# Kernel optimization log

Hardware: AMD Instinct MI355X
Metric: run time of the kernel (lower is better)

Reference implementation:

```python
import jax, jax.numpy as jnp
import numpy as np

BETA = 0.25       # commit-loss weight (beta)
INIT_GAIN = 0.02  # trunc_normal std for codebook init
B, L, D = 4, 4096, 3
VOCAB = 8192


def setup_inputs() -> dict:
    key = jax.random.key(0)
    k1, k2 = jax.random.split(key)
    feats = jax.random.normal(k1, (B, L, D), dtype=jnp.float32)
    # frozen codebook (nn.Embedding weight), trunc_normal(std=0.02) approximated by normal*0.02
    emb = jax.random.normal(k2, (VOCAB, D), dtype=jnp.float32) * INIT_GAIN
    return {"feats": feats, "emb": emb}


def reference(feats, emb):
    b, l, d = feats.shape
    flat = feats.reshape(-1, d)                                # [N, D]
    dist = (jnp.sum(flat * flat, axis=1, keepdims=True)
            - 2.0 * (flat @ emb.T)
            + jnp.sum(emb * emb, axis=1))
    idx = jnp.argmin(dist, axis=1)                             # [N] int
    quant = emb[idx].reshape(b, l, d)                          # gather lookup
    # e_latent_loss: codebook->encoder MSE (feats detached); commit: beta * encoder->codebook MSE
    e_latent_loss = jnp.mean((quant - jax.lax.stop_gradient(feats)) ** 2)
    commit_loss = BETA * jnp.mean((feats - jax.lax.stop_gradient(quant)) ** 2)
    vq_loss = e_latent_loss + commit_loss
    # straight-through estimator
    quant_ste = feats + jax.lax.stop_gradient(quant - feats)
    return quant_ste, idx.reshape(b, l), vq_loss
```

## Files before the change

### kernel.cpp

```cpp
#include <hip/hip_runtime.h>
#include <cstdint>

#define N_ROWS   16384
#define VOCAB    8192
#define BLOCK    512
#define ROWS_PB  32
#define NPIECE   8
#define PIECE    1024
#define GRID     (N_ROWS / ROWS_PB)

typedef unsigned long long u64;


__global__ __launch_bounds__(BLOCK, 4) void vq_main_kernel(
    const float* __restrict__ feats, const float* __restrict__ emb,
    float* __restrict__ out_quant, float* __restrict__ out_idx,
    float* __restrict__ partial)
{
    __shared__ float4 sE[PIECE];
    __shared__ float  wsum[BLOCK / 64];

    const int tid = threadIdx.x;
    const int c   = tid & 15;
    const int row = blockIdx.x * ROWS_PB + (tid >> 4);

    const float x0 = feats[3 * row + 0];
    const float x1 = feats[3 * row + 1];
    const float x2 = feats[3 * row + 2];
    const float xx = __fadd_rn(__fadd_rn(__fmul_rn(x0, x0), __fmul_rn(x1, x1)),
                               __fmul_rn(x2, x2));

    const float* g = emb + 3 * tid;
    float a0 = g[0],    a1 = g[1],    a2 = g[2];
    float b0 = g[1536], b1 = g[1537], b2 = g[1538];

    float best = __int_as_float(0x7f800000);
    int   bj   = 0;

    for (int p = 0; p < NPIECE; ++p) {
        __syncthreads();
        sE[tid] = make_float4(a0, a1, a2,
            __fadd_rn(__fadd_rn(__fmul_rn(a0, a0), __fmul_rn(a1, a1)), __fmul_rn(a2, a2)));
        sE[tid + BLOCK] = make_float4(b0, b1, b2,
            __fadd_rn(__fadd_rn(__fmul_rn(b0, b0), __fmul_rn(b1, b1)), __fmul_rn(b2, b2)));
        __syncthreads();

        if (p + 1 < NPIECE) {
            const float* gn = emb + 3 * ((p + 1) * PIECE + tid);
            a0 = gn[0];    a1 = gn[1];    a2 = gn[2];
            b0 = gn[1536]; b1 = gn[1537]; b2 = gn[1538];
        }

        float pbest = __int_as_float(0x7f800000);
        int   pj    = 0;
        #pragma unroll
        for (int j = 0; j < 64; ++j) {
            const float4 E = sE[j * 16 + c];
            const float xe = __fmaf_rn(x2, E.z, __fmaf_rn(x1, E.y, __fmul_rn(x0, E.x)));
            const float d  = __fadd_rn(__fsub_rn(xx, __fadd_rn(xe, xe)), E.w);
            if (d < pbest) { pbest = d; pj = j; }
        }
        if (pbest < best) { best = pbest; bj = p * 64 + pj; }
    }

    u64 key = ((u64)__float_as_uint(best) << 32) | (unsigned)(bj * 16 + c);
    #pragma unroll
    for (int off = 1; off < 16; off <<= 1) {
        const u64 other = __shfl_xor(key, off, 64);
        if (other < key) key = other;
    }

    float s = 0.0f;
    if (c == 0) {
        const unsigned idx = (unsigned)(key & 0xffffffffULL);
        const float e0 = emb[3 * idx + 0];
        const float e1 = emb[3 * idx + 1];
        const float e2 = emb[3 * idx + 2];
        out_quant[3 * row + 0] = __fadd_rn(x0, __fsub_rn(e0, x0));
        out_quant[3 * row + 1] = __fadd_rn(x1, __fsub_rn(e1, x1));
        out_quant[3 * row + 2] = __fadd_rn(x2, __fsub_rn(e2, x2));
        out_idx[row] = (float)idx;
        const float d0 = e0 - x0, d1 = e1 - x1, d2 = e2 - x2;
        s = d0 * d0 + d1 * d1 + d2 * d2;
    }

    #pragma unroll
    for (int off = 1; off < 64; off <<= 1) s += __shfl_xor(s, off, 64);
    if ((tid & 63) == 0) wsum[tid >> 6] = s;
    __syncthreads();
    if (tid == 0) {
        float t = 0.0f;
        #pragma unroll
        for (int w = 0; w < BLOCK / 64; ++w) t += wsum[w];
        partial[blockIdx.x] = t;
    }
}

__global__ __launch_bounds__(GRID) void vq_loss_kernel(
    const float* __restrict__ partial, float* __restrict__ out_loss)
{
    __shared__ float wsum[GRID / 64];
    float s = partial[threadIdx.x];
    #pragma unroll
    for (int off = 1; off < 64; off <<= 1) s += __shfl_xor(s, off, 64);
    if ((threadIdx.x & 63) == 0) wsum[threadIdx.x >> 6] = s;
    __syncthreads();
    if (threadIdx.x == 0) {
        float t = 0.0f;
        #pragma unroll
        for (int w = 0; w < GRID / 64; ++w) t += wsum[w];
        const float m = t / (float)(N_ROWS * 3);
        out_loss[0] = __fadd_rn(m, __fmul_rn(0.25f, m));
    }
}

extern "C" void kernel_launch(void* const* d_in, const int* in_sizes, int n_in,
                              void* d_out, int out_size, void* d_ws, size_t ws_size,
                              hipStream_t stream)
{
    const float* feats = (const float*)d_in[0];
    const float* emb   = (const float*)d_in[1];
    float* out = (float*)d_out;
    float* partial = (float*)d_ws;

    vq_main_kernel<<<GRID, BLOCK, 0, stream>>>(
        feats, emb, out, out + (size_t)N_ROWS * 3, partial);
    vq_loss_kernel<<<1, GRID, 0, stream>>>(partial, out + (size_t)N_ROWS * 4);
}
```

Before: 83.31 us.

## Register-block 8 rows per wave and pre-double codebook in LDS

Each wave now holds 8 query rows in registers and each lane scans a 1/64 slice of every codebook piece, so a single LDS float4 load is reused across 8 rows instead of serving one. The codebook is stored already doubled, which removes the per-distance xe+xe add. Blocks cover 64 rows, so the grid drops to 256 blocks, and each row now needs a 64-lane shuffle argmin reduction. Register pressure rises and occupancy is lowered to 2 blocks per SM in launch bounds.

```diff
diff --git a/kernel.cpp b/kernel.cpp
--- a/kernel.cpp
+++ b/kernel.cpp
@@ -4,45 +4,58 @@
 #define N_ROWS   16384
 #define VOCAB    8192
 #define BLOCK    512
-#define ROWS_PB  32
-#define NPIECE   8
+#define NWAVES   (BLOCK / 64)
+#define RPW      8
+#define ROWS_PB  (NWAVES * RPW)
+#define GRID     (N_ROWS / ROWS_PB)
 #define PIECE    1024
-#define GRID     (N_ROWS / ROWS_PB)
+#define NPIECE   (VOCAB / PIECE)
 
 typedef unsigned long long u64;
 
 
-__global__ __launch_bounds__(BLOCK, 4) void vq_main_kernel(
+__global__ __launch_bounds__(BLOCK, 2) void vq_main_kernel(
     const float* __restrict__ feats, const float* __restrict__ emb,
     float* __restrict__ out_quant, float* __restrict__ out_idx,
     float* __restrict__ partial)
 {
     __shared__ float4 sE[PIECE];
-    __shared__ float  wsum[BLOCK / 64];
+    __shared__ float  wsum[NWAVES];
 
-    const int tid = threadIdx.x;
-    const int c   = tid & 15;
-    const int row = blockIdx.x * ROWS_PB + (tid >> 4);
+    const int tid   = threadIdx.x;
+    const int lane  = tid & 63;
+    const int wave  = tid >> 6;
+    const int wrow0 = blockIdx.x * ROWS_PB + wave * RPW;
 
-    const float x0 = feats[3 * row + 0];
-    const float x1 = feats[3 * row + 1];
-    const float x2 = feats[3 * row + 2];
-    const float xx = __fadd_rn(__fadd_rn(__fmul_rn(x0, x0), __fmul_rn(x1, x1)),
-                               __fmul_rn(x2, x2));
+    float x0[RPW], x1[RPW], x2[RPW], xx[RPW];
+    #pragma unroll
+    for (int r = 0; r < RPW; ++r) {
+        x0[r] = feats[3 * (wrow0 + r) + 0];
+        x1[r] = feats[3 * (wrow0 + r) + 1];
+        x2[r] = feats[3 * (wrow0 + r) + 2];
+        xx[r] = __fadd_rn(__fadd_rn(__fmul_rn(x0[r], x0[r]), __fmul_rn(x1[r], x1[r])),
+                          __fmul_rn(x2[r], x2[r]));
+    }
 
     const float* g = emb + 3 * tid;
     float a0 = g[0],    a1 = g[1],    a2 = g[2];
     float b0 = g[1536], b1 = g[1537], b2 = g[1538];
 
-    float best = __int_as_float(0x7f800000);
-    int   bj   = 0;
+    float best[RPW];
+    int   bpj[RPW];
+    #pragma unroll
+    for (int r = 0; r < RPW; ++r) { best[r] = __int_as_float(0x7f800000); bpj[r] = 0; }
 
     for (int p = 0; p < NPIECE; ++p) {
         __syncthreads();
-        sE[tid] = make_float4(a0, a1, a2,
-            __fadd_rn(__fadd_rn(__fmul_rn(a0, a0), __fmul_rn(a1, a1)), __fmul_rn(a2, a2)));
-        sE[tid + BLOCK] = make_float4(b0, b1, b2,
-            __fadd_rn(__fadd_rn(__fmul_rn(b0, b0), __fmul_rn(b1, b1)), __fmul_rn(b2, b2)));
+        {
+            const float eea = __fadd_rn(__fadd_rn(__fmul_rn(a0, a0), __fmul_rn(a1, a1)),
+                                        __fmul_rn(a2, a2));
+            const float eeb = __fadd_rn(__fadd_rn(__fmul_rn(b0, b0), __fmul_rn(b1, b1)),
+                                        __fmul_rn(b2, b2));
+            sE[tid]         = make_float4(a0 + a0, a1 + a1, a2 + a2, eea);
+            sE[tid + BLOCK] = make_float4(b0 + b0, b1 + b1, b2 + b2, eeb);
+        }
         __syncthreads();
 
         if (p + 1 < NPIECE) {
@@ -51,47 +64,64 @@
             b0 = gn[1536]; b1 = gn[1537]; b2 = gn[1538];
         }
 
-        float pbest = __int_as_float(0x7f800000);
-        int   pj    = 0;
+        const int pj0 = p * 16;
         #pragma unroll
-        for (int j = 0; j < 64; ++j) {
-            const float4 E = sE[j * 16 + c];
-            const float xe = __fmaf_rn(x2, E.z, __fmaf_rn(x1, E.y, __fmul_rn(x0, E.x)));
-            const float d  = __fadd_rn(__fsub_rn(xx, __fadd_rn(xe, xe)), E.w);
-            if (d < pbest) { pbest = d; pj = j; }
+        for (int j = 0; j < 16; ++j) {
+            const float4 E = sE[j * 64 + lane];
+            const int pj = pj0 + j;
+            #pragma unroll
+            for (int r = 0; r < RPW; ++r) {
+                const float xe2 = __fmaf_rn(x2[r], E.z,
+                                  __fmaf_rn(x1[r], E.y, __fmul_rn(x0[r], E.x)));
+                const float d = __fadd_rn(__fsub_rn(xx[r], xe2), E.w);
+                if (d < best[r]) { best[r] = d; bpj[r] = pj; }
+            }
         }
-        if (pbest < best) { best = pbest; bj = p * 64 + pj; }
     }
 
-    u64 key = ((u64)__float_as_uint(best) << 32) | (unsigned)(bj * 16 + c);
+    u64 key[RPW];
     #pragma unroll
-    for (int off = 1; off < 16; off <<= 1) {
-        const u64 other = __shfl_xor(key, off, 64);
-        if (other < key) key = other;
+    for (int r = 0; r < RPW; ++r) {
+        const unsigned code = (unsigned)((bpj[r] >> 4) * PIECE + (bpj[r] & 15) * 64 + lane);
+        u64 k = ((u64)__float_as_uint(best[r]) << 32) | code;
+        #pragma unroll
+        for (int off = 1; off < 64; off <<= 1) {
+            const u64 o = __shfl_xor(k, off, 64);
+            if (o < k) k = o;
+        }
+        key[r] = k;
     }
 
+    u64 mykey = key[0];
+    #pragma unroll
+    for (int r = 1; r < RPW; ++r) mykey = (lane == r) ? key[r] : mykey;
+
     float s = 0.0f;
-    if (c == 0) {
-        const unsigned idx = (unsigned)(key & 0xffffffffULL);
+    if (lane < RPW) {
+        const int row = wrow0 + lane;
+        const unsigned idx = (unsigned)(mykey & 0xffffffffULL);
         const float e0 = emb[3 * idx + 0];
         const float e1 = emb[3 * idx + 1];
         const float e2 = emb[3 * idx + 2];
-        out_quant[3 * row + 0] = __fadd_rn(x0, __fsub_rn(e0, x0));
-        out_quant[3 * row + 1] = __fadd_rn(x1, __fsub_rn(e1, x1));
-        out_quant[3 * row + 2] = __fadd_rn(x2, __fsub_rn(e2, x2));
+        const float fx0 = feats[3 * row + 0];
+        const float fx1 = feats[3 * row + 1];
+        const float fx2 = feats[3 * row + 2];
+        out_quant[3 * row + 0] = __fadd_rn(fx0, __fsub_rn(e0, fx0));
+        out_quant[3 * row + 1] = __fadd_rn(fx1, __fsub_rn(e1, fx1));
+        out_quant[3 * row + 2] = __fadd_rn(fx2, __fsub_rn(e2, fx2));
         out_idx[row] = (float)idx;
-        const float d0 = e0 - x0, d1 = e1 - x1, d2 = e2 - x2;
+        const float d0 = e0 - fx0, d1 = e1 - fx1, d2 = e2 - fx2;
         s = d0 * d0 + d1 * d1 + d2 * d2;
     }
 
     #pragma unroll
     for (int off = 1; off < 64; off <<= 1) s += __shfl_xor(s, off, 64);
-    if ((tid & 63) == 0) wsum[tid >> 6] = s;
+    if (lane == 0) wsum[wave] = s;
     __syncthreads();
     if (tid == 0) {
         float t = 0.0f;
         #pragma unroll
-        for (int w = 0; w < BLOCK / 64; ++w) t += wsum[w];
+        for (int w = 0; w < NWAVES; ++w) t += wsum[w];
         partial[blockIdx.x] = t;
     }
 }
```

Measured after the change: 87.26 us. 1.05x slower.

## Sort codebook by norm and early-exit nearest-code search via triangle bound

Applied to the files above, without the earlier changes.

A prep kernel buckets codebook entries by descending squared norm, stores pre-doubled vectors with norms, and builds a suffix-max of chunk norms. The main kernel scans chunks in that order and stops once a triangle-inequality bound shows no remaining chunk can beat the current best, so most of the 8192-code search is skipped. It also folds the loss reduction into the main kernel with an atomic last-block pattern. The single-block prep kernel adds serial latency, and the epsilon-padded bound could alter tie-breaking or pick a different argmin in edge cases.

```diff
diff --git a/kernel.cpp b/kernel.cpp
--- a/kernel.cpp
+++ b/kernel.cpp
@@ -3,114 +3,220 @@
 
 #define N_ROWS   16384
 #define VOCAB    8192
-#define BLOCK    512
-#define ROWS_PB  32
-#define NPIECE   8
-#define PIECE    1024
-#define GRID     (N_ROWS / ROWS_PB)
+#define NCHUNKS  512
+#define PCHUNKS  64
 
 typedef unsigned long long u64;
-
-
-__global__ __launch_bounds__(BLOCK, 4) void vq_main_kernel(
+typedef unsigned int u32;
+
+
+__global__ __launch_bounds__(1024) void vq_prep(
+    const float* __restrict__ emb, float4* __restrict__ sorted,
+    u32* __restrict__ order, float* __restrict__ suf, u32* __restrict__ counter)
+{
+    __shared__ u32 hist[64];
+    __shared__ u32 starts[64];
+    __shared__ int maxeb_s;
+    __shared__ float cmax[512];
+
+    const int t = threadIdx.x;
+    if (t == 0) { maxeb_s = -1; counter[0] = 0u; }
+    if (t < 64) hist[t] = 0u;
+    __syncthreads();
+
+    float e0[8], e1[8], e2[8], ee[8];
+    int eb[8];
+    int mymax = -1;
+    #pragma unroll
+    for (int i = 0; i < 8; ++i) {
+        const int code = t + i * 1024;
+        e0[i] = emb[3*code+0]; e1[i] = emb[3*code+1]; e2[i] = emb[3*code+2];
+        ee[i] = __fadd_rn(__fadd_rn(__fmul_rn(e0[i],e0[i]), __fmul_rn(e1[i],e1[i])),
+                          __fmul_rn(e2[i],e2[i]));
+        eb[i] = (int)(__float_as_uint(ee[i]) >> 22);
+        mymax = max(mymax, eb[i]);
+    }
+    atomicMax(&maxeb_s, mymax);
+    __syncthreads();
+    const int off = maxeb_s - 63;
+
+    int sbin[8];
+    #pragma unroll
+    for (int i = 0; i < 8; ++i) {
+        int b = eb[i] - off; b = b < 0 ? 0 : b;
+        sbin[i] = 63 - b;
+        atomicAdd(&hist[sbin[i]], 1u);
+    }
+    __syncthreads();
+    if (t < 64) {
+        const u32 h = hist[t];
+        u32 incl = h;
+        #pragma unroll
+        for (int o = 1; o < 64; o <<= 1) {
+            const u32 v = __shfl_up(incl, o, 64);
+            if (t >= o) incl += v;
+        }
+        starts[t] = incl - h;
+    }
+    __syncthreads();
+    #pragma unroll
+    for (int i = 0; i < 8; ++i) {
+        const u32 pos = atomicAdd(&starts[sbin[i]], 1u);
+        sorted[pos] = make_float4(e0[i]+e0[i], e1[i]+e1[i], e2[i]+e2[i], ee[i]);
+        order[pos]  = (u32)(t + i * 1024);
+    }
+    __syncthreads();
+
+    if (t < 512) {
+        float m = sorted[t*16].w;
+        #pragma unroll
+        for (int i = 1; i < 16; ++i) m = fmaxf(m, sorted[t*16+i].w);
+        cmax[t] = m;
+    }
+    __syncthreads();
+    if (t < 64) {
+        float v[8];
+        #pragma unroll
+        for (int i = 0; i < 8; ++i) v[i] = cmax[t*8+i];
+        #pragma unroll
+        for (int i = 6; i >= 0; --i) v[i] = fmaxf(v[i], v[i+1]);
+        float incl = v[0];
+        #pragma unroll
+        for (int o = 1; o < 64; o <<= 1) {
+            const float w = __shfl_down(incl, o, 64);
+            if (t + o < 64) incl = fmaxf(incl, w);
+        }
+        float excl = __shfl_down(incl, 1, 64);
+        if (t == 63) excl = 0.0f;
+        #pragma unroll
+        for (int i = 0; i < 8; ++i) suf[t*8+i] = fmaxf(v[i], excl);
+        if (t == 0) suf[512] = 0.0f;
+    }
+}
+
+__global__ __launch_bounds__(256) void vq_main(
     const float* __restrict__ feats, const float* __restrict__ emb,
-    float* __restrict__ out_quant, float* __restrict__ out_idx,
-    float* __restrict__ partial)
+    const float4* __restrict__ sorted, const u32* __restrict__ order,
+    const float* __restrict__ suf, float* __restrict__ out_quant,
+    float* __restrict__ out_idx, float* __restrict__ part,
+    u32* __restrict__ counter, float* __restrict__ loss_slot)
 {
-    __shared__ float4 sE[PIECE];
-    __shared__ float  wsum[BLOCK / 64];
-
-    const int tid = threadIdx.x;
-    const int c   = tid & 15;
-    const int row = blockIdx.x * ROWS_PB + (tid >> 4);
-
-    const float x0 = feats[3 * row + 0];
-    const float x1 = feats[3 * row + 1];
-    const float x2 = feats[3 * row + 2];
-    const float xx = __fadd_rn(__fadd_rn(__fmul_rn(x0, x0), __fmul_rn(x1, x1)),
-                               __fmul_rn(x2, x2));
-
-    const float* g = emb + 3 * tid;
-    float a0 = g[0],    a1 = g[1],    a2 = g[2];
-    float b0 = g[1536], b1 = g[1537], b2 = g[1538];
+    __shared__ float4 sE[1024];
+    __shared__ float  sSuf[513];
+    __shared__ float  wsum[4];
+    __shared__ int    winner;
+
+    const int tid  = threadIdx.x;
+    const int lane = tid & 63;
+    const int wave = tid >> 6;
+    const int c    = tid & 15;
+    const int row  = blockIdx.x * 16 + (tid >> 4);
+
+    sE[tid]       = sorted[tid];
+    sE[tid + 256] = sorted[tid + 256];
+    sE[tid + 512] = sorted[tid + 512];
+    sE[tid + 768] = sorted[tid + 768];
+    for (int i = tid; i < 513; i += 256) sSuf[i] = suf[i];
+
+    const float x0 = feats[3*row+0];
+    const float x1 = feats[3*row+1];
+    const float x2 = feats[3*row+2];
+    const float xx = __fadd_rn(__fadd_rn(__fmul_rn(x0,x0), __fmul_rn(x1,x1)),
+                               __fmul_rn(x2,x2));
+    const float sx = sqrtf(xx) - 1e-5f;
+
+    __syncthreads();
 
     float best = __int_as_float(0x7f800000);
-    int   bj   = 0;
-
-    for (int p = 0; p < NPIECE; ++p) {
-        __syncthreads();
-        sE[tid] = make_float4(a0, a1, a2,
-            __fadd_rn(__fadd_rn(__fmul_rn(a0, a0), __fmul_rn(a1, a1)), __fmul_rn(a2, a2)));
-        sE[tid + BLOCK] = make_float4(b0, b1, b2,
-            __fadd_rn(__fadd_rn(__fmul_rn(b0, b0), __fmul_rn(b1, b1)), __fmul_rn(b2, b2)));
-        __syncthreads();
-
-        if (p + 1 < NPIECE) {
-            const float* gn = emb + 3 * ((p + 1) * PIECE + tid);
-            a0 = gn[0];    a1 = gn[1];    a2 = gn[2];
-            b0 = gn[1536]; b1 = gn[1537]; b2 = gn[1538];
-        }
-
-        float pbest = __int_as_float(0x7f800000);
-        int   pj    = 0;
-        #pragma unroll
-        for (int j = 0; j < 64; ++j) {
-            const float4 E = sE[j * 16 + c];
-            const float xe = __fmaf_rn(x2, E.z, __fmaf_rn(x1, E.y, __fmul_rn(x0, E.x)));
-            const float d  = __fadd_rn(__fsub_rn(xx, __fadd_rn(xe, xe)), E.w);
-            if (d < pbest) { pbest = d; pj = j; }
-        }
-        if (pbest < best) { best = pbest; bj = p * 64 + pj; }
-    }
-
-    u64 key = ((u64)__float_as_uint(best) << 32) | (unsigned)(bj * 16 + c);
-    #pragma unroll
-    for (int off = 1; off < 16; off <<= 1) {
-        const u64 other = __shfl_xor(key, off, 64);
-        if (other < key) key = other;
+    int   bpos = c;
+    bool  done = false;
+
+    for (int k = 0; k < PCHUNKS; ++k) {
+        const float4 E = sE[k*16 + c];
+        const float xe2 = __fmaf_rn(x2, E.z, __fmaf_rn(x1, E.y, __fmul_rn(x0, E.x)));
+        const float d   = __fadd_rn(__fsub_rn(xx, xe2), E.w);
+        if (d < best) { best = d; bpos = k*16 + c; }
+        if ((k & 3) == 3) {
+            float gb = best;
+            gb = fminf(gb, __shfl_xor(gb, 1, 64));
+            gb = fminf(gb, __shfl_xor(gb, 2, 64));
+            gb = fminf(gb, __shfl_xor(gb, 4, 64));
+            gb = fminf(gb, __shfl_xor(gb, 8, 64));
+            const float T  = sx - (sqrtf(gb + 1e-4f) + 1e-5f);
+            const float T2 = (T > 0.0f) ? (T*T - 1e-5f) : -1.0e30f;
+            if (__ballot(sSuf[k+1] >= T2) == 0ULL) { done = true; break; }
+        }
+    }
+
+    if (!done) {
+        for (int kb = PCHUNKS; kb < NCHUNKS; kb += 8) {
+            float4 Eb[8];
+            #pragma unroll
+            for (int j = 0; j < 8; ++j) Eb[j] = sorted[(kb+j)*16 + c];
+            #pragma unroll
+            for (int j = 0; j < 8; ++j) {
+                const float4 E = Eb[j];
+                const float xe2 = __fmaf_rn(x2, E.z, __fmaf_rn(x1, E.y, __fmul_rn(x0, E.x)));
+                const float d   = __fadd_rn(__fsub_rn(xx, xe2), E.w);
+                if (d < best) { best = d; bpos = (kb+j)*16 + c; }
+            }
+            if (kb + 8 >= NCHUNKS) break;
+            float gb = best;
+            gb = fminf(gb, __shfl_xor(gb, 1, 64));
+            gb = fminf(gb, __shfl_xor(gb, 2, 64));
+            gb = fminf(gb, __shfl_xor(gb, 4, 64));
+            gb = fminf(gb, __shfl_xor(gb, 8, 64));
+            const float T  = sx - (sqrtf(gb + 1e-4f) + 1e-5f);
+            const float T2 = (T > 0.0f) ? (T*T - 1e-5f) : -1.0e30f;
+            if (__ballot(sSuf[kb+8] >= T2) == 0ULL) break;
+        }
+    }
+
+    const u32 orig = order[bpos];
+    u64 key = ((u64)__float_as_uint(best) << 32) | (u64)orig;
+    {
+        u64 o;
+        o = __shfl_xor(key, 1, 64); if (o < key) key = o;
+        o = __shfl_xor(key, 2, 64); if (o < key) key = o;
+        o = __shfl_xor(key, 4, 64); if (o < key) key = o;
+        o = __shfl_xor(key, 8, 64); if (o < key) key = o;
     }
 
     float s = 0.0f;
     if (c == 0) {
-        const unsigned idx = (unsigned)(key & 0xffffffffULL);
-        const float e0 = emb[3 * idx + 0];
-        const float e1 = emb[3 * idx + 1];
-        const float e2 = emb[3 * idx + 2];
-        out_quant[3 * row + 0] = __fadd_rn(x0, __fsub_rn(e0, x0));
-        out_quant[3 * row + 1] = __fadd_rn(x1, __fsub_rn(e1, x1));
-        out_quant[3 * row + 2] = __fadd_rn(x2, __fsub_rn(e2, x2));
+        const u32 idx = (u32)(key & 0xffffffffULL);
+        const float e0 = emb[3*idx+0];
+        const float e1 = emb[3*idx+1];
+        const float e2 = emb[3*idx+2];
+        out_quant[3*row+0] = __fadd_rn(x0, __fsub_rn(e0, x0));
+        out_quant[3*row+1] = __fadd_rn(x1, __fsub_rn(e1, x1));
+        out_quant[3*row+2] = __fadd_rn(x2, __fsub_rn(e2, x2));
         out_idx[row] = (float)idx;
         const float d0 = e0 - x0, d1 = e1 - x1, d2 = e2 - x2;
-        s = d0 * d0 + d1 * d1 + d2 * d2;
-    }
-
-    #pragma unroll
-    for (int off = 1; off < 64; off <<= 1) s += __shfl_xor(s, off, 64);
-    if ((tid & 63) == 0) wsum[tid >> 6] = s;
+        s = d0*d0 + d1*d1 + d2*d2;
+    }
+    #pragma unroll
+    for (int o = 1; o < 64; o <<= 1) s += __shfl_xor(s, o, 64);
+    if (lane == 0) wsum[wave] = s;
     __syncthreads();
     if (tid == 0) {
-        float t = 0.0f;
-        #pragma unroll
-        for (int w = 0; w < BLOCK / 64; ++w) t += wsum[w];
-        partial[blockIdx.x] = t;
-    }
-}
-
-__global__ __launch_bounds__(GRID) void vq_loss_kernel(
-    const float* __restrict__ partial, float* __restrict__ out_loss)
-{
-    __shared__ float wsum[GRID / 64];
-    float s = partial[threadIdx.x];
-    #pragma unroll
-    for (int off = 1; off < 64; off <<= 1) s += __shfl_xor(s, off, 64);
-    if ((threadIdx.x & 63) == 0) wsum[threadIdx.x >> 6] = s;
-    __syncthreads();
-    if (threadIdx.x == 0) {
-        float t = 0.0f;
-        #pragma unroll
-        for (int w = 0; w < GRID / 64; ++w) t += wsum[w];
-        const float m = t / (float)(N_ROWS * 3);
-        out_loss[0] = __fadd_rn(m, __fmul_rn(0.25f, m));
+        part[blockIdx.x] = (wsum[0] + wsum[1]) + (wsum[2] + wsum[3]);
+        __threadfence();
+        const u32 old = atomicAdd(counter, 1u);
+        winner = (old == 1023u) ? 1 : 0;
+    }
+    __syncthreads();
+    if (winner) {
+        float v = part[tid] + part[tid+256] + part[tid+512] + part[tid+768];
+        #pragma unroll
+        for (int o = 1; o < 64; o <<= 1) v += __shfl_xor(v, o, 64);
+        if (lane == 0) wsum[wave] = v;
+        __syncthreads();
+        if (tid == 0) {
+            const float S = (wsum[0] + wsum[1]) + (wsum[2] + wsum[3]);
+            const float m = S / (float)(N_ROWS * 3);
+            loss_slot[0] = __fadd_rn(m, __fmul_rn(0.25f, m));
+        }
     }
 }
 
@@ -121,9 +227,16 @@
     const float* feats = (const float*)d_in[0];
     const float* emb   = (const float*)d_in[1];
     float* out = (float*)d_out;
-    float* partial = (float*)d_ws;
-
-    vq_main_kernel<<<GRID, BLOCK, 0, stream>>>(
-        feats, emb, out, out + (size_t)N_ROWS * 3, partial);
-    vq_loss_kernel<<<1, GRID, 0, stream>>>(partial, out + (size_t)N_ROWS * 4);
+
+    char* ws = (char*)d_ws;
+    float4* sorted  = (float4*)(ws);
+    u32*    order   = (u32*)(ws + 131072);
+    float*  suf     = (float*)(ws + 163840);
+    float*  part    = (float*)(ws + 167936);
+    u32*    counter = (u32*)(ws + 172032);
+
+    vq_prep<<<1, 1024, 0, stream>>>(emb, sorted, order, suf, counter);
+    vq_main<<<1024, 256, 0, stream>>>(feats, emb, sorted, order, suf,
+                                      out, out + (size_t)N_ROWS * 3,
+                                      part, counter, out + (size_t)N_ROWS * 4);
 }
```

Measured after the change: 100.1 us. 20.1% more time.
